# Optimization experiments

Measured on AMD Instinct MI355X. Metric: run time of the kernel, lower is better.

## Reference

```python
import jax, jax.numpy as jnp
import numpy as np

K = 20          # neighbors
EPS = 1e-5      # BatchNorm eps
SLOPE = 0.2     # LeakyReLU negative slope


def setup_inputs() -> dict:
    key = jax.random.key(0)
    ks = jax.random.split(key, 6)
    B, C, N, O = 8, 3, 4096, 64
    x = jax.random.normal(ks[0], (B, C, N), dtype=jnp.float32)
    W = jax.random.normal(ks[1], (O, 2 * C), dtype=jnp.float32) * 0.1  # conv1x1 weight, bias=False
    gamma = 1.0 + 0.1 * jax.random.normal(ks[2], (O,), dtype=jnp.float32)
    beta = 0.1 * jax.random.normal(ks[3], (O,), dtype=jnp.float32)
    mean = 0.1 * jax.random.normal(ks[4], (O,), dtype=jnp.float32)
    var = jax.random.uniform(ks[5], (O,), dtype=jnp.float32, minval=0.5, maxval=1.5)
    return {"x": x, "W": W, "gamma": gamma, "beta": beta, "mean": mean, "var": var}


def reference(x, W, gamma, beta, mean, var):
    # x: [B, C, N]
    B, C, N = x.shape
    xt = jnp.swapaxes(x, 1, 2)                                   # [B, N, C]
    xx = jnp.sum(x * x, axis=1)                                  # [B, N]
    pd = 2.0 * jnp.einsum('bnc,bmc->bnm', xt, xt) - xx[:, :, None] - xx[:, None, :]
    _, idx = jax.lax.top_k(pd, K)                                # [B, N, K] nearest neighbors
    # gather neighbor features per batch
    feat = jax.vmap(lambda f, i: f[i])(xt, idx)                  # [B, N, K, C]
    center = xt[:, :, None, :]                                   # [B, N, 1, C]
    edge = jnp.concatenate(
        [feat - center, jnp.broadcast_to(center, feat.shape)], axis=-1)  # [B, N, K, 2C]
    # 1x1 conv == channel matmul
    y = jnp.einsum('bnkc,oc->bnko', edge, W)                     # [B, N, K, O]
    inv = gamma / jnp.sqrt(var + EPS)                            # fused inference BatchNorm
    y = y * inv + (beta - mean * inv)
    y = jnp.where(y >= 0, y, SLOPE * y)                          # LeakyReLU(0.2)
    y = jnp.max(y, axis=2)                                       # max over k -> [B, N, O]
    return jnp.swapaxes(y, 1, 2)                                 # [B, O, N]
```

## Files before the change

### kernel.cpp

```cpp
#include <hip/hip_runtime.h>
#include <math.h>

#define NPTS 4096
#define KNN  20
#define NOUT 64
#define WPB  8
#define QPW  2
#define QBLK (WPB * QPW)
#define BLKT (WPB * 64)
#define PCAP 96
#define HALF 2048

__device__ __forceinline__ unsigned ord32(float f) {
    unsigned u = __float_as_uint(f);
    int m = ((int)u) >> 31;
    return u ^ ((unsigned)m | 0x80000000u);
}

__device__ __forceinline__ int mbcnt64(unsigned long long m) {
    return __builtin_amdgcn_mbcnt_hi((unsigned)(m >> 32),
           __builtin_amdgcn_mbcnt_lo((unsigned)m, 0));
}

__global__ __launch_bounds__(256) void pack_kernel(const float* __restrict__ x,
                                                   float4* __restrict__ xq) {
    const int i = blockIdx.x * 256 + threadIdx.x;
    const int b = i >> 12, j = i & (NPTS - 1);
    const float* xb = x + (size_t)b * 3 * NPTS;
    const float a0 = xb[j], a1 = xb[NPTS + j], a2 = xb[2 * NPTS + j];
    xq[i] = make_float4(a0, a1, a2, -fmaf(a0, a0, fmaf(a1, a1, a2 * a2)));
}

__global__ __launch_bounds__(BLKT, 6) void edgeconv_kernel(
    const float4* __restrict__ xq,
    const float* __restrict__ Wm,
    const float* __restrict__ gamma,
    const float* __restrict__ beta,
    const float* __restrict__ mean,
    const float* __restrict__ var,
    float* __restrict__ out)
{
    const int bid = blockIdx.x;
    const int b   = bid >> 8;
    const int n0  = (bid & 255) * QBLK;
    const int t    = threadIdx.x;
    const int lane = t & 63;
    const int w    = t >> 6;

    __shared__ float4 tile[HALF];
    __shared__ unsigned long long pool[QBLK * PCAP];
    __shared__ unsigned idxs[QBLK][KNN];
    __shared__ float outT[NOUT * (QBLK + 1)];
    __shared__ int cnt[QBLK];

    const float4* xqb = xq + (size_t)b * NPTS;

    if (lane < QPW) cnt[QPW * w + lane] = 0;

    #pragma unroll
    for (int k2 = 0; k2 < HALF / BLKT; ++k2) {
        const int c = t + k2 * BLKT;
        tile[c] = xqb[c];
    }
    __syncthreads();

    const int na = __builtin_amdgcn_readfirstlane(n0 + QPW * w);
    const int nb = na + 1;
    const float4 pva = xqb[na];
    const float4 pvb = xqb[nb];
    const float qa0 = 2.f * pva.x, qa1 = 2.f * pva.y, qa2 = 2.f * pva.z;
    const float qb0 = 2.f * pvb.x, qb1 = 2.f * pvb.y, qb2 = 2.f * pvb.z;

    float vma = -INFINITY, vmb = -INFINITY;
    #pragma unroll
    for (int g = 0; g < 4; ++g) {
        float4 cc[8];
        #pragma unroll
        for (int u = 0; u < 8; ++u) cc[u] = tile[(g * 8 + u) * 64 + lane];
        #pragma unroll
        for (int u = 0; u < 8; ++u) {
            const float ea = fmaf(qa0, cc[u].x, fmaf(qa1, cc[u].y, fmaf(qa2, cc[u].z, cc[u].w)));
            const float eb = fmaf(qb0, cc[u].x, fmaf(qb1, cc[u].y, fmaf(qb2, cc[u].z, cc[u].w)));
            vma = fmaxf(vma, ea);
            vmb = fmaxf(vmb, eb);
        }
    }

    float Ta, Tb;
    {
        float va = vma, vb = vmb;
        #pragma unroll
        for (int k = 2; k <= 64; k <<= 1) {
            #pragma unroll
            for (int j = k >> 1; j > 0; j >>= 1) {
                const float oa = __shfl_xor(va, j, 64);
                const float ob = __shfl_xor(vb, j, 64);
                const bool keep_min = ((lane & j) == 0) == ((lane & k) != 0);
                va = keep_min ? fminf(va, oa) : fmaxf(va, oa);
                vb = keep_min ? fminf(vb, ob) : fmaxf(vb, ob);
            }
        }
        Ta = __shfl(va, 19, 64);
        Tb = __shfl(vb, 19, 64);
    }

    const int invl = (NPTS - 1) - lane;
    int* cnta = &cnt[QPW * w];
    int* cntb = &cnt[QPW * w + 1];
    unsigned long long* poola = pool + (QPW * w) * PCAP;
    unsigned long long* poolb = pool + (QPW * w + 1) * PCAP;

    #pragma unroll
    for (int g = 0; g < 4; ++g) {
        float4 cc[8];
        #pragma unroll
        for (int u = 0; u < 8; ++u) cc[u] = tile[(g * 8 + u) * 64 + lane];
        #pragma unroll
        for (int u = 0; u < 8; ++u) {
            const float ea = fmaf(qa0, cc[u].x, fmaf(qa1, cc[u].y, fmaf(qa2, cc[u].z, cc[u].w)));
            const float eb = fmaf(qb0, cc[u].x, fmaf(qb1, cc[u].y, fmaf(qb2, cc[u].z, cc[u].w)));
            const unsigned tag = (unsigned)(invl - (g * 8 + u) * 64);
            if (ea >= Ta) {
                const int pos = atomicAdd(cnta, 1);
                if (pos < PCAP)
                    poola[pos] = ((unsigned long long)ord32(ea) << 32) | tag;
            }
            if (eb >= Tb) {
                const int pos = atomicAdd(cntb, 1);
                if (pos < PCAP)
                    poolb[pos] = ((unsigned long long)ord32(eb) << 32) | tag;
            }
        }
    }

    #pragma unroll
    for (int g = 4; g < 8; ++g) {
        float4 cc[8];
        #pragma unroll
        for (int u = 0; u < 8; ++u) cc[u] = xqb[(g * 8 + u) * 64 + lane];
        #pragma unroll
        for (int u = 0; u < 8; ++u) {
            const float ea = fmaf(qa0, cc[u].x, fmaf(qa1, cc[u].y, fmaf(qa2, cc[u].z, cc[u].w)));
            const float eb = fmaf(qb0, cc[u].x, fmaf(qb1, cc[u].y, fmaf(qb2, cc[u].z, cc[u].w)));
            const unsigned tag = (unsigned)(invl - (g * 8 + u) * 64);
            if (ea >= Ta) {
                const int pos = atomicAdd(cnta, 1);
                if (pos < PCAP)
                    poola[pos] = ((unsigned long long)ord32(ea) << 32) | tag;
            }
            if (eb >= Tb) {
                const int pos = atomicAdd(cntb, 1);
                if (pos < PCAP)
                    poolb[pos] = ((unsigned long long)ord32(eb) << 32) | tag;
            }
        }
    }

    #pragma unroll
    for (int q = 0; q < QPW; ++q) {
        const int pr = QPW * w + q;
        unsigned long long* pl = pool + (size_t)pr * PCAP;
        const int cntw = __builtin_amdgcn_readfirstlane(cnt[pr]);
        const int cnt_ = (cntw < PCAP) ? cntw : PCAP;

        unsigned long long kk = 0ull;
        if (lane < cnt_) kk = pl[lane];

        if (cnt_ <= 64) {
            const unsigned key = (unsigned)(kk >> 32);
            unsigned v = key;
            #pragma unroll
            for (int k = 2; k <= 64; k <<= 1) {
                #pragma unroll
                for (int j = k >> 1; j > 0; j >>= 1) {
                    const unsigned o = (unsigned)__shfl_xor((int)v, j, 64);
                    const bool keep_min = ((lane & j) == 0) == ((lane & k) != 0);
                    v = keep_min ? min(v, o) : max(v, o);
                }
            }
            const unsigned K20 = (unsigned)__shfl((int)v, 19, 64);
            const unsigned long long ge = __ballot(key >= K20);
            if (__popcll(ge) == KNN) {
                if (key >= K20) idxs[pr][mbcnt64(ge)] = (unsigned)kk;
            } else {
                unsigned long long key64 = kk;
                #pragma unroll
                for (int k = 2; k <= 64; k <<= 1) {
                    #pragma unroll
                    for (int j = k >> 1; j > 0; j >>= 1) {
                        const unsigned long long o = __shfl_xor(key64, j, 64);
                        const bool keep_min = ((lane & j) == 0) == ((lane & k) != 0);
                        const unsigned long long mn = (key64 < o) ? key64 : o;
                        const unsigned long long mx = (key64 < o) ? o : key64;
                        key64 = keep_min ? mn : mx;
                    }
                }
                if (lane < KNN) idxs[pr][lane] = (unsigned)key64;
            }
        } else {
            for (int r = 0; r < KNN; ++r) {
                unsigned long long bk = 0ull; int bp = -1;
                for (int i = lane; i < cnt_; i += 64) {
                    const unsigned long long e = pl[i];
                    if (e > bk) { bk = e; bp = i; }
                }
                unsigned long long rb = bk;
                #pragma unroll
                for (int s = 32; s > 0; s >>= 1) {
                    const unsigned long long o = __shfl_xor(rb, s, 64);
                    if (o > rb) rb = o;
                }
                if (bk == rb && bp >= 0) pl[bp] = 0ull;
                if (lane == 0) idxs[pr][r] = (unsigned)rb;
            }
        }
    }

    const unsigned myidxa = idxs[QPW * w][(lane < KNN) ? lane : 0];
    const unsigned myidxb = idxs[QPW * w + 1][(lane < KNN) ? lane : 0];

    const int o = lane;
    const float iv   = gamma[o] / sqrtf(var[o] + 1e-5f);
    const float bias = beta[o] - mean[o] * iv;
    const float* Wr = Wm + o * 6;
    const float w0p = Wr[0] * iv, w1p = Wr[1] * iv, w2p = Wr[2] * iv;
    const float w3p = Wr[3] * iv, w4p = Wr[4] * iv, w5p = Wr[5] * iv;
    const float basea = fmaf(w3p, pva.x, fmaf(w4p, pva.y, fmaf(w5p, pva.z, bias)));
    const float base2a = basea - fmaf(w0p, pva.x, fmaf(w1p, pva.y, w2p * pva.z));
    const float baseb = fmaf(w3p, pvb.x, fmaf(w4p, pvb.y, fmaf(w5p, pvb.z, bias)));
    const float base2b = baseb - fmaf(w0p, pvb.x, fmaf(w1p, pvb.y, w2p * pvb.z));

    float besta = -INFINITY, bestb = -INFINITY;
    #pragma unroll
    for (int k = 0; k < KNN; ++k) {
        const int lka = __builtin_amdgcn_readlane((int)myidxa, k);
        const int lkb = __builtin_amdgcn_readlane((int)myidxb, k);
        const int gia = __builtin_amdgcn_readfirstlane((NPTS - 1) - lka);
        const int gib = __builtin_amdgcn_readfirstlane((NPTS - 1) - lkb);
        const float4 fa = xqb[gia];
        const float4 fb = xqb[gib];
        float ya = fmaf(w0p, fa.x, fmaf(w1p, fa.y, fmaf(w2p, fa.z, base2a)));
        float yb = fmaf(w0p, fb.x, fmaf(w1p, fb.y, fmaf(w2p, fb.z, base2b)));
        ya = fmaxf(ya, 0.2f * ya);
        yb = fmaxf(yb, 0.2f * yb);
        besta = fmaxf(besta, ya);
        bestb = fmaxf(bestb, yb);
    }

    outT[o * (QBLK + 1) + QPW * w]     = besta;
    outT[o * (QBLK + 1) + QPW * w + 1] = bestb;
    __syncthreads();

    if (t < NOUT * 4) {
        const int oo = t >> 2, seg = t & 3;
        const int sb = oo * (QBLK + 1) + seg * 4;
        float4 vv;
        vv.x = outT[sb + 0]; vv.y = outT[sb + 1];
        vv.z = outT[sb + 2]; vv.w = outT[sb + 3];
        *(float4*)(out + ((size_t)b * NOUT + oo) * NPTS + n0 + seg * 4) = vv;
    }
}

extern "C" void kernel_launch(void* const* d_in, const int* in_sizes, int n_in,
                              void* d_out, int out_size, void* d_ws, size_t ws_size,
                              hipStream_t stream) {
    const float* x     = (const float*)d_in[0];
    const float* Wm    = (const float*)d_in[1];
    const float* gamma = (const float*)d_in[2];
    const float* beta  = (const float*)d_in[3];
    const float* mean  = (const float*)d_in[4];
    const float* var   = (const float*)d_in[5];
    float* out = (float*)d_out;
    float4* xq = (float4*)d_ws;

    const int B = in_sizes[0] / (3 * NPTS);
    pack_kernel<<<B * NPTS / 256, 256, 0, stream>>>(x, xq);
    const int nblocks = B * (NPTS / QBLK);
    edgeconv_kernel<<<nblocks, BLKT, 0, stream>>>(xq, Wm, gamma, beta, mean, var, out);
}
```

Before: 144.2 us.

## Replace bitonic sorts with ballot radix-select and fuse tile load with threshold scan

The per-wave threshold for candidate filtering is now found by a 32-step ballot/popcount radix select on ordered keys instead of a full 64-lane bitonic sort. Final top-20 selection also uses radix select over up to 128 pool entries, with a tie-break on tags, which removes the serial fallback path for overflowing pools. The shared tile load is fused with the first half of the max-scan so the first barrier moves later, and the idxs/outT shared arrays are aliased onto the pool to shrink LDS and raise occupancy. The cost is extra ballots per bit step and a more complex tie-handling path.

```diff
diff --git a/kernel.cpp b/kernel.cpp
--- a/kernel.cpp
+++ b/kernel.cpp
@@ -16,7 +16,10 @@
     int m = ((int)u) >> 31;
     return u ^ ((unsigned)m | 0x80000000u);
 }
-
+__device__ __forceinline__ float iord32(unsigned r) {
+    unsigned u = (r & 0x80000000u) ? (r ^ 0x80000000u) : ~r;
+    return __uint_as_float(u);
+}
 __device__ __forceinline__ int mbcnt64(unsigned long long m) {
     return __builtin_amdgcn_mbcnt_hi((unsigned)(m >> 32),
            __builtin_amdgcn_mbcnt_lo((unsigned)m, 0));
@@ -49,34 +52,36 @@
 
     __shared__ float4 tile[HALF];
     __shared__ unsigned long long pool[QBLK * PCAP];
-    __shared__ unsigned idxs[QBLK][KNN];
-    __shared__ float outT[NOUT * (QBLK + 1)];
     __shared__ int cnt[QBLK];
 
     const float4* xqb = xq + (size_t)b * NPTS;
 
     if (lane < QPW) cnt[QPW * w + lane] = 0;
+
+    const int na = __builtin_amdgcn_readfirstlane(n0 + QPW * w);
+    const float4 pva = xqb[na];
+    const float4 pvb = xqb[na + 1];
+    const float qa0 = 2.f * pva.x, qa1 = 2.f * pva.y, qa2 = 2.f * pva.z;
+    const float qb0 = 2.f * pvb.x, qb1 = 2.f * pvb.y, qb2 = 2.f * pvb.z;
+
+    float vma = -INFINITY, vmb = -INFINITY;
 
     #pragma unroll
     for (int k2 = 0; k2 < HALF / BLKT; ++k2) {
         const int c = t + k2 * BLKT;
-        tile[c] = xqb[c];
-    }
-    __syncthreads();
-
-    const int na = __builtin_amdgcn_readfirstlane(n0 + QPW * w);
-    const int nb = na + 1;
-    const float4 pva = xqb[na];
-    const float4 pvb = xqb[nb];
-    const float qa0 = 2.f * pva.x, qa1 = 2.f * pva.y, qa2 = 2.f * pva.z;
-    const float qb0 = 2.f * pvb.x, qb1 = 2.f * pvb.y, qb2 = 2.f * pvb.z;
-
-    float vma = -INFINITY, vmb = -INFINITY;
-    #pragma unroll
-    for (int g = 0; g < 4; ++g) {
+        const float4 cc = xqb[c];
+        tile[c] = cc;
+        const float ea = fmaf(qa0, cc.x, fmaf(qa1, cc.y, fmaf(qa2, cc.z, cc.w)));
+        const float eb = fmaf(qb0, cc.x, fmaf(qb1, cc.y, fmaf(qb2, cc.z, cc.w)));
+        vma = fmaxf(vma, ea);
+        vmb = fmaxf(vmb, eb);
+    }
+
+    #pragma unroll
+    for (int g = 4; g < 8; ++g) {
         float4 cc[8];
         #pragma unroll
-        for (int u = 0; u < 8; ++u) cc[u] = tile[(g * 8 + u) * 64 + lane];
+        for (int u = 0; u < 8; ++u) cc[u] = xqb[(g * 8 + u) * 64 + lane];
         #pragma unroll
         for (int u = 0; u < 8; ++u) {
             const float ea = fmaf(qa0, cc[u].x, fmaf(qa1, cc[u].y, fmaf(qa2, cc[u].z, cc[u].w)));
@@ -86,29 +91,29 @@
         }
     }
 
-    float Ta, Tb;
+    unsigned Ka = 0, Kb = 0;
     {
-        float va = vma, vb = vmb;
-        #pragma unroll
-        for (int k = 2; k <= 64; k <<= 1) {
-            #pragma unroll
-            for (int j = k >> 1; j > 0; j >>= 1) {
-                const float oa = __shfl_xor(va, j, 64);
-                const float ob = __shfl_xor(vb, j, 64);
-                const bool keep_min = ((lane & j) == 0) == ((lane & k) != 0);
-                va = keep_min ? fminf(va, oa) : fmaxf(va, oa);
-                vb = keep_min ? fminf(vb, ob) : fmaxf(vb, ob);
-            }
-        }
-        Ta = __shfl(va, 19, 64);
-        Tb = __shfl(vb, 19, 64);
-    }
+        const unsigned ka = ord32(vma), kb = ord32(vmb);
+        #pragma unroll
+        for (int bit = 31; bit >= 0; --bit) {
+            const unsigned pa = Ka | (1u << bit);
+            const unsigned pb = Kb | (1u << bit);
+            const int ca = __popcll(__ballot(ka >= pa));
+            const int cb = __popcll(__ballot(kb >= pb));
+            if (ca >= KNN) Ka = pa;
+            if (cb >= KNN) Kb = pb;
+        }
+    }
+    const float Tfa = iord32(Ka);
+    const float Tfb = iord32(Kb);
+
+    __syncthreads();
 
     const int invl = (NPTS - 1) - lane;
     int* cnta = &cnt[QPW * w];
     int* cntb = &cnt[QPW * w + 1];
-    unsigned long long* poola = pool + (QPW * w) * PCAP;
-    unsigned long long* poolb = pool + (QPW * w + 1) * PCAP;
+    unsigned long long* poola = pool + (size_t)(QPW * w) * PCAP;
+    unsigned long long* poolb = pool + (size_t)(QPW * w + 1) * PCAP;
 
     #pragma unroll
     for (int g = 0; g < 4; ++g) {
@@ -120,12 +125,12 @@
             const float ea = fmaf(qa0, cc[u].x, fmaf(qa1, cc[u].y, fmaf(qa2, cc[u].z, cc[u].w)));
             const float eb = fmaf(qb0, cc[u].x, fmaf(qb1, cc[u].y, fmaf(qb2, cc[u].z, cc[u].w)));
             const unsigned tag = (unsigned)(invl - (g * 8 + u) * 64);
-            if (ea >= Ta) {
+            if (ea >= Tfa) {
                 const int pos = atomicAdd(cnta, 1);
                 if (pos < PCAP)
                     poola[pos] = ((unsigned long long)ord32(ea) << 32) | tag;
             }
-            if (eb >= Tb) {
+            if (eb >= Tfb) {
                 const int pos = atomicAdd(cntb, 1);
                 if (pos < PCAP)
                     poolb[pos] = ((unsigned long long)ord32(eb) << 32) | tag;
@@ -143,12 +148,12 @@
             const float ea = fmaf(qa0, cc[u].x, fmaf(qa1, cc[u].y, fmaf(qa2, cc[u].z, cc[u].w)));
             const float eb = fmaf(qb0, cc[u].x, fmaf(qb1, cc[u].y, fmaf(qb2, cc[u].z, cc[u].w)));
             const unsigned tag = (unsigned)(invl - (g * 8 + u) * 64);
-            if (ea >= Ta) {
+            if (ea >= Tfa) {
                 const int pos = atomicAdd(cnta, 1);
                 if (pos < PCAP)
                     poola[pos] = ((unsigned long long)ord32(ea) << 32) | tag;
             }
-            if (eb >= Tb) {
+            if (eb >= Tfb) {
                 const int pos = atomicAdd(cntb, 1);
                 if (pos < PCAP)
                     poolb[pos] = ((unsigned long long)ord32(eb) << 32) | tag;
@@ -156,68 +161,55 @@
         }
     }
 
+    unsigned myidx[QPW];
     #pragma unroll
     for (int q = 0; q < QPW; ++q) {
         const int pr = QPW * w + q;
         unsigned long long* pl = pool + (size_t)pr * PCAP;
-        const int cntw = __builtin_amdgcn_readfirstlane(cnt[pr]);
-        const int cnt_ = (cntw < PCAP) ? cntw : PCAP;
-
-        unsigned long long kk = 0ull;
-        if (lane < cnt_) kk = pl[lane];
-
-        if (cnt_ <= 64) {
-            const unsigned key = (unsigned)(kk >> 32);
-            unsigned v = key;
+        int cw = __builtin_amdgcn_readfirstlane(cnt[pr]);
+        if (cw > PCAP) cw = PCAP;
+
+        const unsigned long long e0 = (lane < cw) ? pl[lane] : 0ull;
+        const unsigned long long e1 = (lane + 64 < cw) ? pl[lane + 64] : 0ull;
+        const unsigned k0 = (unsigned)(e0 >> 32), t0 = (unsigned)e0;
+        const unsigned k1 = (unsigned)(e1 >> 32), t1 = (unsigned)e1;
+
+        unsigned K = 0;
+        #pragma unroll
+        for (int bit = 31; bit >= 0; --bit) {
+            const unsigned p = K | (1u << bit);
+            const int c = __popcll(__ballot(k0 >= p)) + __popcll(__ballot(k1 >= p));
+            if (c >= KNN) K = p;
+        }
+
+        unsigned long long g0 = __ballot(k0 > K);
+        unsigned long long g1 = __ballot(k1 > K);
+        const int m = __popcll(g0) + __popcll(g1);
+        unsigned long long q0 = __ballot(k0 == K);
+        unsigned long long q1 = __ballot(k1 == K);
+        const int r = KNN - m;
+        if (__popcll(q0) + __popcll(q1) > r) {
+            unsigned TT = 0;
             #pragma unroll
-            for (int k = 2; k <= 64; k <<= 1) {
-                #pragma unroll
-                for (int j = k >> 1; j > 0; j >>= 1) {
-                    const unsigned o = (unsigned)__shfl_xor((int)v, j, 64);
-                    const bool keep_min = ((lane & j) == 0) == ((lane & k) != 0);
-                    v = keep_min ? min(v, o) : max(v, o);
-                }
-            }
-            const unsigned K20 = (unsigned)__shfl((int)v, 19, 64);
-            const unsigned long long ge = __ballot(key >= K20);
-            if (__popcll(ge) == KNN) {
-                if (key >= K20) idxs[pr][mbcnt64(ge)] = (unsigned)kk;
-            } else {
-                unsigned long long key64 = kk;
-                #pragma unroll
-                for (int k = 2; k <= 64; k <<= 1) {
-                    #pragma unroll
-                    for (int j = k >> 1; j > 0; j >>= 1) {
-                        const unsigned long long o = __shfl_xor(key64, j, 64);
-                        const bool keep_min = ((lane & j) == 0) == ((lane & k) != 0);
-                        const unsigned long long mn = (key64 < o) ? key64 : o;
-                        const unsigned long long mx = (key64 < o) ? o : key64;
-                        key64 = keep_min ? mn : mx;
-                    }
-                }
-                if (lane < KNN) idxs[pr][lane] = (unsigned)key64;
-            }
-        } else {
-            for (int r = 0; r < KNN; ++r) {
-                unsigned long long bk = 0ull; int bp = -1;
-                for (int i = lane; i < cnt_; i += 64) {
-                    const unsigned long long e = pl[i];
-                    if (e > bk) { bk = e; bp = i; }
-                }
-                unsigned long long rb = bk;
-                #pragma unroll
-                for (int s = 32; s > 0; s >>= 1) {
-                    const unsigned long long o = __shfl_xor(rb, s, 64);
-                    if (o > rb) rb = o;
-                }
-                if (bk == rb && bp >= 0) pl[bp] = 0ull;
-                if (lane == 0) idxs[pr][r] = (unsigned)rb;
-            }
-        }
-    }
-
-    const unsigned myidxa = idxs[QPW * w][(lane < KNN) ? lane : 0];
-    const unsigned myidxb = idxs[QPW * w + 1][(lane < KNN) ? lane : 0];
+            for (int bit = 11; bit >= 0; --bit) {
+                const unsigned p = TT | (1u << bit);
+                const int c = __popcll(__ballot(k0 == K && t0 >= p)) +
+                              __popcll(__ballot(k1 == K && t1 >= p));
+                if (c >= r) TT = p;
+            }
+            q0 = __ballot(k0 == K && t0 >= TT);
+            q1 = __ballot(k1 == K && t1 >= TT);
+        }
+
+        unsigned* idxq = (unsigned*)pl;
+        if ((g0 >> lane) & 1) idxq[mbcnt64(g0)] = t0;
+        if ((g1 >> lane) & 1) idxq[__popcll(g0) + mbcnt64(g1)] = t1;
+        if ((q0 >> lane) & 1) idxq[m + mbcnt64(q0)] = t0;
+        if ((q1 >> lane) & 1) idxq[m + __popcll(q0) + mbcnt64(q1)] = t1;
+        myidx[q] = idxq[(lane < KNN) ? lane : 0];
+    }
+
+    __syncthreads();
 
     const int o = lane;
     const float iv   = gamma[o] / sqrtf(var[o] + 1e-5f);
@@ -233,8 +225,8 @@
     float besta = -INFINITY, bestb = -INFINITY;
     #pragma unroll
     for (int k = 0; k < KNN; ++k) {
-        const int lka = __builtin_amdgcn_readlane((int)myidxa, k);
-        const int lkb = __builtin_amdgcn_readlane((int)myidxb, k);
+        const int lka = __builtin_amdgcn_readlane((int)myidx[0], k);
+        const int lkb = __builtin_amdgcn_readlane((int)myidx[1], k);
         const int gia = __builtin_amdgcn_readfirstlane((NPTS - 1) - lka);
         const int gib = __builtin_amdgcn_readfirstlane((NPTS - 1) - lkb);
         const float4 fa = xqb[gia];
@@ -247,6 +239,7 @@
         bestb = fmaxf(bestb, yb);
     }
 
+    float* outT = (float*)pool;
     outT[o * (QBLK + 1) + QPW * w]     = besta;
     outT[o * (QBLK + 1) + QPW * w + 1] = bestb;
     __syncthreads();
```

Result: faster. 130.6 us (-9.4%).
